# Optimization experiments

Measured on AMD Instinct MI355X. Metric: run time of the kernel, lower is better.

The kernel has to match this reference:

```python
import jax, jax.numpy as jnp
import numpy as np

N = 12000
E = 384000
F_IN, F_HID, F_OUT = 4, 50, 1433
NEG_SLOPE = 0.2  # PyG GATConv default leaky_relu slope


def gat_conv(x, W, a_src, a_dst, b, src, dst):
    """PyG GATConv (heads=1, concat=True) with self-loops already appended.
    x: [N, Fin], W: [Fin, Fout], a_src/a_dst/b: [Fout], src/dst: [E']."""
    h = x @ W                                   # [N, Fout]
    al = h @ a_src                              # [N] per-source logit part
    ar = h @ a_dst                              # [N] per-target logit part
    e = jax.nn.leaky_relu(al[src] + ar[dst], NEG_SLOPE)   # [E'] edge logits
    # segment softmax over edges grouped by destination node
    m = jax.ops.segment_max(e, dst, num_segments=N)       # [N]
    ex = jnp.exp(e - m[dst])
    s = jax.ops.segment_sum(ex, dst, num_segments=N)      # [N]
    alpha = ex / s[dst]                         # [E'] (self-loops => s > 0)
    out = jax.ops.segment_sum(alpha[:, None] * h[src], dst, num_segments=N)
    return out + b


def setup_inputs() -> dict:
    key = jax.random.key(0)
    ks = jax.random.split(key, 10)
    x = jax.random.normal(ks[0], (N, F_IN), dtype=jnp.float32)
    edge_index = jax.random.randint(ks[1], (2, E), 0, N, dtype=jnp.int32)
    # Glorot-ish init for params
    W1 = jax.random.normal(ks[2], (F_IN, F_HID), dtype=jnp.float32) / np.sqrt(F_IN)
    a_src1 = jax.random.normal(ks[3], (F_HID,), dtype=jnp.float32) / np.sqrt(F_HID)
    a_dst1 = jax.random.normal(ks[4], (F_HID,), dtype=jnp.float32) / np.sqrt(F_HID)
    b1 = jnp.zeros((F_HID,), dtype=jnp.float32)
    W2 = jax.random.normal(ks[5], (F_HID, F_OUT), dtype=jnp.float32) / np.sqrt(F_HID)
    a_src2 = jax.random.normal(ks[6], (F_OUT,), dtype=jnp.float32) / np.sqrt(F_OUT)
    a_dst2 = jax.random.normal(ks[7], (F_OUT,), dtype=jnp.float32) / np.sqrt(F_OUT)
    b2 = jnp.zeros((F_OUT,), dtype=jnp.float32)
    return {"x": x, "edge_index": edge_index, "W1": W1, "a_src1": a_src1,
            "a_dst1": a_dst1, "b1": b1, "W2": W2, "a_src2": a_src2,
            "a_dst2": a_dst2, "b2": b2}


def reference(x, edge_index, W1, a_src1, a_dst1, b1, W2, a_src2, a_dst2, b2):
    # PyG GATConv adds self-loops by default
    loops = jnp.arange(N, dtype=edge_index.dtype)
    src = jnp.concatenate([edge_index[0], loops])
    dst = jnp.concatenate([edge_index[1], loops])
    h = jax.nn.relu(gat_conv(x, W1, a_src1, a_dst1, b1, src, dst))
    h = jax.nn.relu(gat_conv(h, W2, a_src2, a_dst2, b2, src, dst))
    adj_pred = jax.nn.sigmoid(h @ h.T)          # InnerProductDecoder.forward_all
    return (adj_pred, edge_index)
```

## Files before the change

kernel.cpp:

```cpp
#include <hip/hip_runtime.h>
#include <hip/hip_bf16.h>

#define NNODES 12000
#define NEDGES 384000
#define NETOT  (NEDGES + NNODES)
#define FIN    4
#define FHID   50
#define FOUT   1433
#define KP     1440
#define MP     12032
#define NTILE  (MP / 128)
#define NTRI   (NTILE * (NTILE + 1) / 2)
#define NEG_SLOPE 0.2f

typedef __hip_bfloat16 bf16_t;
typedef __bf16 bf16x8 __attribute__((ext_vector_type(8)));
typedef float f32x4 __attribute__((ext_vector_type(4)));
typedef float f32x2 __attribute__((ext_vector_type(2)));

__device__ __forceinline__ float  b2f(bf16_t h) { return __bfloat162float(h); }
__device__ __forceinline__ bf16_t f2b(float f)  { return __float2bfloat16(f); }
__device__ __forceinline__ unsigned short f2bu(float f) { bf16_t h = f2b(f); return *(unsigned short*)&h; }

__global__ void k_init(int* __restrict__ deg, bf16_t* __restrict__ h2) {
    int i = blockIdx.x * blockDim.x + threadIdx.x;
    int stride = gridDim.x * blockDim.x;
    for (int v = i; v < NNODES; v += stride) deg[v] = 1;
    const size_t padN = (size_t)(MP - NNODES) * KP;
    for (size_t t = i; t < padN; t += stride) h2[(size_t)NNODES * KP + t] = f2b(0.f);
}

__global__ void k_count(const int* __restrict__ ei, int* __restrict__ deg) {
    int i = blockIdx.x * blockDim.x + threadIdx.x;
    if (i < NEDGES) atomicAdd(&deg[ei[NEDGES + i]], 1);
}

__global__ __launch_bounds__(1024) void k_scan(const int* __restrict__ deg,
                                               int* __restrict__ rowptr,
                                               int* __restrict__ cursor) {
    __shared__ int wsum[16];
    const int tid = threadIdx.x, lane = tid & 63, wv = tid >> 6;
    const int base = tid * 12;
    int pref[12];
    int s = 0;
#pragma unroll
    for (int u = 0; u < 12; ++u) {
        int idx = base + u;
        int d = (idx < NNODES) ? deg[idx] : 0;
        pref[u] = s;
        s += d;
    }
    int sc = s;
#pragma unroll
    for (int o = 1; o < 64; o <<= 1) {
        int t2 = __shfl_up(sc, o, 64);
        if (lane >= o) sc += t2;
    }
    if (lane == 63) wsum[wv] = sc;
    __syncthreads();
    if (wv == 0 && lane < 16) {
        int mine = wsum[lane];
        int scw = mine;
#pragma unroll
        for (int o = 1; o < 16; o <<= 1) {
            int t3 = __shfl_up(scw, o, 64);
            if (lane >= o) scw += t3;
        }
        wsum[lane] = scw - mine;
    }
    __syncthreads();
    const int pre = wsum[wv] + (sc - s);
#pragma unroll
    for (int u = 0; u < 12; ++u) {
        int idx = base + u;
        if (idx < NNODES) {
            int p = pre + pref[u];
            rowptr[idx] = p;
            cursor[idx] = p;
        }
    }
    if (tid == 1023) rowptr[NNODES] = pre + s;
}

__global__ void k_fill(const int* __restrict__ ei, int* __restrict__ cursor,
                       int* __restrict__ csrc, float* __restrict__ outbase) {
    int i = blockIdx.x * blockDim.x + threadIdx.x;
    if (i < NETOT) {
        int s, d;
        if (i < NEDGES) { s = ei[i]; d = ei[NEDGES + i]; }
        else            { s = d = i - NEDGES; }
        int pos = atomicAdd(&cursor[d], 1);
        csrc[pos] = s;
    }
    if (i < 2 * NEDGES)
        outbase[(size_t)NNODES * (size_t)NNODES + (size_t)i] = (float)ei[i];
}

__global__ __launch_bounds__(256) void k_linear1(
        const bf16_t* __restrict__ x, const bf16_t* __restrict__ W1,
        const bf16_t* __restrict__ as1, const bf16_t* __restrict__ ad1,
        float* __restrict__ h1pre, float* __restrict__ al, float* __restrict__ ar) {
    __shared__ float sW[FIN * FHID];
    __shared__ float sa[FHID], sdl[FHID];
    int tid = threadIdx.x;
    if (tid < FIN * FHID) sW[tid] = b2f(W1[tid]);
    if (tid < FHID) { sa[tid] = b2f(as1[tid]); sdl[tid] = b2f(ad1[tid]); }
    __syncthreads();
    int i = blockIdx.x * 256 + tid;
    if (i >= NNODES) return;
    float x0 = b2f(x[i * 4 + 0]), x1 = b2f(x[i * 4 + 1]);
    float x2 = b2f(x[i * 4 + 2]), x3 = b2f(x[i * 4 + 3]);
    float hal = 0.f, har = 0.f;
    for (int j = 0; j < FHID; ++j) {
        float h = x0 * sW[j] + x1 * sW[FHID + j] + x2 * sW[2 * FHID + j] + x3 * sW[3 * FHID + j];
        h1pre[(size_t)i * FHID + j] = h;
        hal += h * sa[j];
        har += h * sdl[j];
    }
    al[i] = hal; ar[i] = har;
}

__global__ __launch_bounds__(256) void k_agg1(
        const float* __restrict__ h1pre, const float* __restrict__ al, const float* __restrict__ ar,
        const int* __restrict__ rowptr, const int* __restrict__ csrc,
        const bf16_t* __restrict__ b1, float* __restrict__ h1) {
    const int wv = threadIdx.x >> 6, lane = threadIdx.x & 63;
    const int v = blockIdx.x * 4 + wv;
    const int s0 = rowptr[v], s1 = rowptr[v + 1];
    const float arv = ar[v];
    float acc = 0.f, ssum = 0.f;
    for (int base = s0; base < s1; base += 64) {
        int e = base + lane;
        float w = 0.f; int si = 0;
        if (e < s1) {
            si = csrc[e];
            float l = al[si] + arv;
            l = l > 0.f ? l : NEG_SLOPE * l;
            w = __expf(l);
        }
        ssum += w;
        int cnt = min(64, s1 - base);
#pragma unroll 4
        for (int j = 0; j < cnt; ++j) {
            float wj = __shfl(w, j, 64);
            int   sj = __shfl(si, j, 64);
            if (lane < FHID) acc += wj * h1pre[(size_t)sj * FHID + lane];
        }
    }
#pragma unroll
    for (int o = 32; o; o >>= 1) ssum += __shfl_xor(ssum, o, 64);
    if (lane < FHID) {
        float o2 = acc / ssum + b2f(b1[lane]);
        h1[(size_t)v * FHID + lane] = fmaxf(o2, 0.f);
    }
}

__global__ __launch_bounds__(256) void k_linear2(
        const float* __restrict__ h1, const bf16_t* __restrict__ W2,
        const bf16_t* __restrict__ as2, const bf16_t* __restrict__ ad2,
        unsigned char* __restrict__ h2pre, float* __restrict__ al2, float* __restrict__ ar2) {
    int v0 = blockIdx.x * 4, tid = threadIdx.x;
    __shared__ float sh[4][FHID];
    if (tid < 4 * FHID) sh[tid / FHID][tid % FHID] = h1[(size_t)v0 * FHID + tid];
    __syncthreads();
    float pal[4] = {0.f, 0.f, 0.f, 0.f}, par[4] = {0.f, 0.f, 0.f, 0.f};
#pragma unroll
    for (int i = 0; i < 3; ++i) {
        int f0 = i * 512 + 2 * tid;
        if (f0 < KP) {
            float d0[4] = {0.f, 0.f, 0.f, 0.f}, d1[4] = {0.f, 0.f, 0.f, 0.f};
            bool ok0 = f0 < FOUT, ok1 = f0 + 1 < FOUT;
            if (ok0) {
                int f1 = ok1 ? f0 + 1 : f0;
#pragma unroll 10
                for (int k = 0; k < FHID; ++k) {
                    float w0 = b2f(W2[k * FOUT + f0]);
                    float w1 = b2f(W2[k * FOUT + f1]);
#pragma unroll
                    for (int c = 0; c < 4; ++c) {
                        d0[c] += sh[c][k] * w0;
                        d1[c] += sh[c][k] * w1;
                    }
                }
                if (!ok1) { d1[0] = d1[1] = d1[2] = d1[3] = 0.f; }
                float sa0 = b2f(as2[f0]), sd0 = b2f(ad2[f0]);
                float sa1 = ok1 ? b2f(as2[f0 + 1]) : 0.f;
                float sd1 = ok1 ? b2f(ad2[f0 + 1]) : 0.f;
#pragma unroll
                for (int c = 0; c < 4; ++c) {
                    pal[c] += d0[c] * sa0 + d1[c] * sa1;
                    par[c] += d0[c] * sd0 + d1[c] * sd1;
                }
            }
#pragma unroll
            for (int c = 0; c < 4; ++c) {
                int pk = __builtin_amdgcn_cvt_pk_fp8_f32(d0[c], d1[c], 0, false);
                *(unsigned short*)(h2pre + (size_t)(v0 + c) * KP + f0) = (unsigned short)pk;
            }
        }
    }
#pragma unroll
    for (int off = 32; off; off >>= 1)
#pragma unroll
        for (int c = 0; c < 4; ++c) {
            pal[c] += __shfl_xor(pal[c], off, 64);
            par[c] += __shfl_xor(par[c], off, 64);
        }
    __shared__ float rA[4][4], rB[4][4];
    int wave = tid >> 6, lane = tid & 63;
    if (lane == 0)
#pragma unroll
        for (int c = 0; c < 4; ++c) { rA[wave][c] = pal[c]; rB[wave][c] = par[c]; }
    __syncthreads();
    if (tid < 4) {
        al2[v0 + tid] = rA[0][tid] + rA[1][tid] + rA[2][tid] + rA[3][tid];
        ar2[v0 + tid] = rB[0][tid] + rB[1][tid] + rB[2][tid] + rB[3][tid];
    }
}

__global__ __launch_bounds__(256) void k_agg2(
        const unsigned char* __restrict__ h2pre, const float* __restrict__ al, const float* __restrict__ ar,
        const int* __restrict__ rowptr, const int* __restrict__ csrc,
        const bf16_t* __restrict__ bias2, bf16_t* __restrict__ h2) {
    int v = blockIdx.x, tid = threadIdx.x;
    int s0 = rowptr[v], s1 = rowptr[v + 1];
    float arv = ar[v];
    int wave = tid >> 6, lane = tid & 63;

    float acc[8] = {0.f, 0.f, 0.f, 0.f, 0.f, 0.f, 0.f, 0.f};
    float ssum = 0.f;
    __shared__ float sw[256];
    __shared__ int ssrc[256];
    __shared__ float red[4];
    const bool act = tid < (KP / 8);
    for (int base = s0; base < s1; base += 256) {
        int e = base + tid;
        float w = 0.f; int si = 0;
        if (e < s1) {
            si = csrc[e];
            float l = al[si] + arv;
            l = l > 0.f ? l : NEG_SLOPE * l;
            w = __expf(l);
        }
        ssum += w;
        sw[tid] = w; ssrc[tid] = si;
        __syncthreads();
        int cnt = min(256, s1 - base);
        if (act) {
#pragma unroll 8
            for (int j = 0; j < cnt; ++j) {
                float wj = sw[j];
                const uint2* hp = (const uint2*)(h2pre + (size_t)ssrc[j] * KP);
                uint2 p = hp[tid];
                f32x2 e0 = __builtin_amdgcn_cvt_pk_f32_fp8(p.x, false);
                f32x2 e1 = __builtin_amdgcn_cvt_pk_f32_fp8(p.x, true);
                f32x2 e2 = __builtin_amdgcn_cvt_pk_f32_fp8(p.y, false);
                f32x2 e3 = __builtin_amdgcn_cvt_pk_f32_fp8(p.y, true);
                acc[0] += wj * e0.x; acc[1] += wj * e0.y;
                acc[2] += wj * e1.x; acc[3] += wj * e1.y;
                acc[4] += wj * e2.x; acc[5] += wj * e2.y;
                acc[6] += wj * e3.x; acc[7] += wj * e3.y;
            }
        }
        __syncthreads();
    }
#pragma unroll
    for (int off = 32; off; off >>= 1) ssum += __shfl_xor(ssum, off, 64);
    if (lane == 0) red[wave] = ssum;
    __syncthreads();
    float inv = 1.f / (red[0] + red[1] + red[2] + red[3]);

    if (act) {
        int fb = 8 * tid;
        unsigned short o[8];
#pragma unroll
        for (int t = 0; t < 8; ++t) {
            int f = fb + t;
            o[t] = f2bu((f < FOUT) ? fmaxf(acc[t] * inv + b2f(bias2[f]), 0.f) : 0.f);
        }
        uint4 pk;
        pk.x = (unsigned)o[0] | ((unsigned)o[1] << 16);
        pk.y = (unsigned)o[2] | ((unsigned)o[3] << 16);
        pk.z = (unsigned)o[4] | ((unsigned)o[5] << 16);
        pk.w = (unsigned)o[6] | ((unsigned)o[7] << 16);
        *(uint4*)(h2 + (size_t)v * KP + fb) = pk;
    }
}

__global__ __launch_bounds__(256) void k_gemm_sig(const bf16_t* __restrict__ Hm,
                                                  float* __restrict__ out) {
    int t = blockIdx.x;
    int by = (int)((2 * NTILE + 1 - sqrtf((float)(2 * NTILE + 1) * (2 * NTILE + 1) - 8.0f * t)) * 0.5f);
    if (by < 0) by = 0;
    if (by > NTILE - 1) by = NTILE - 1;
    while (by + 1 < NTILE && (by + 1) * NTILE - ((by + 1) * by) / 2 <= t) ++by;
    while (by > 0 && by * NTILE - (by * (by - 1)) / 2 > t) --by;
    int bx = by + (t - (by * NTILE - (by * (by - 1)) / 2));

    __shared__ __align__(16) bf16_t As[128 * 32];
    __shared__ __align__(16) bf16_t Bs[128 * 32];
    const int tid = threadIdx.x;
    const int wave = tid >> 6;
    const int lane = tid & 63;
    const int rowA0 = by * 128;
    const int rowB0 = bx * 128;

    const int sRow  = wave * 16 + (lane >> 2);
    const int sSlot = (lane & 3) ^ ((lane >> 2) & 3);
    const bf16_t* gA = Hm + (size_t)(rowA0 + sRow) * KP + sSlot * 8;
    const bf16_t* gB = Hm + (size_t)(rowB0 + sRow) * KP + sSlot * 8;

    f32x4 acc[4][4] = {};

    const int wrow = wave >> 1, wcol = wave & 1;
    const int r = lane & 15, q = lane >> 4;
    const int rslot = q ^ (r & 3);
    const __bf16* Asb = (const __bf16*)As;
    const __bf16* Bsb = (const __bf16*)Bs;

    for (int kt = 0; kt < KP / 32; ++kt) {
        const int k0 = kt * 32;
#pragma unroll
        for (int c = 0; c < 2; ++c) {
            __builtin_amdgcn_global_load_lds(
                (const __attribute__((address_space(1))) void*)(gA + (size_t)c * 64 * KP + k0),
                (__attribute__((address_space(3))) void*)((char*)As + c * 4096 + wave * 1024),
                16, 0, 0);
            __builtin_amdgcn_global_load_lds(
                (const __attribute__((address_space(1))) void*)(gB + (size_t)c * 64 * KP + k0),
                (__attribute__((address_space(3))) void*)((char*)Bs + c * 4096 + wave * 1024),
                16, 0, 0);
        }
        __syncthreads();
        bf16x8 af[4], bfr[4];
#pragma unroll
        for (int mi = 0; mi < 4; ++mi)
            af[mi] = *(const bf16x8*)(Asb + ((wrow * 64 + mi * 16 + r) * 32 + rslot * 8));
#pragma unroll
        for (int ni = 0; ni < 4; ++ni)
            bfr[ni] = *(const bf16x8*)(Bsb + ((wcol * 64 + ni * 16 + r) * 32 + rslot * 8));
#pragma unroll
        for (int mi = 0; mi < 4; ++mi)
#pragma unroll
            for (int ni = 0; ni < 4; ++ni)
                acc[mi][ni] = __builtin_amdgcn_mfma_f32_16x16x32_bf16(af[mi], bfr[ni], acc[mi][ni], 0, 0, 0);
        __syncthreads();
    }

#pragma unroll
    for (int mi = 0; mi < 4; ++mi) {
        const int row0 = rowA0 + wrow * 64 + mi * 16 + q * 4;
#pragma unroll
        for (int ni = 0; ni < 4; ++ni) {
            const int col = rowB0 + wcol * 64 + ni * 16 + r;
            if (col < NNODES && row0 < NNODES) {
                f32x4 s;
#pragma unroll
                for (int r2 = 0; r2 < 4; ++r2)
                    s[r2] = 1.f / (1.f + __expf(-acc[mi][ni][r2]));
#pragma unroll
                for (int r2 = 0; r2 < 4; ++r2)
                    out[(size_t)(row0 + r2) * NNODES + col] = s[r2];
                if (bx != by)
                    *(f32x4*)(out + (size_t)col * NNODES + row0) = s;
            }
        }
    }
}

extern "C" void kernel_launch(void* const* d_in, const int* in_sizes, int n_in,
                              void* d_out, int out_size, void* d_ws, size_t ws_size,
                              hipStream_t stream) {
    const bf16_t* x   = (const bf16_t*)d_in[0];
    const int*    ei  = (const int*)d_in[1];
    const bf16_t* W1  = (const bf16_t*)d_in[2];
    const bf16_t* as1 = (const bf16_t*)d_in[3];
    const bf16_t* ad1 = (const bf16_t*)d_in[4];
    const bf16_t* b1  = (const bf16_t*)d_in[5];
    const bf16_t* W2  = (const bf16_t*)d_in[6];
    const bf16_t* as2 = (const bf16_t*)d_in[7];
    const bf16_t* ad2 = (const bf16_t*)d_in[8];
    const bf16_t* b2  = (const bf16_t*)d_in[9];
    float* out = (float*)d_out;

    char* obuf = (char*)d_out;
    size_t off = 0;
    auto carve = [&](size_t bytes) {
        char* p = obuf + off;
        off += (bytes + 255) & ~(size_t)255;
        return p;
    };
    float* h1pre  = (float*)carve((size_t)NNODES * FHID * 4);
    float* al1    = (float*)carve((size_t)NNODES * 4);
    float* ar1    = (float*)carve((size_t)NNODES * 4);
    float* h1     = (float*)carve((size_t)NNODES * FHID * 4);
    float* al2    = (float*)carve((size_t)NNODES * 4);
    float* ar2    = (float*)carve((size_t)NNODES * 4);
    int*   deg    = (int*)carve((size_t)NNODES * 4);
    int*   rowptr = (int*)carve((size_t)(NNODES + 1) * 4);
    int*   cursor = (int*)carve((size_t)NNODES * 4);
    int*   csrc   = (int*)carve((size_t)NETOT * 4);
    unsigned char* h2pre = (unsigned char*)carve((size_t)NNODES * KP);
    bf16_t* h2 = (bf16_t*)d_ws;
    (void)ws_size; (void)in_sizes; (void)n_in; (void)out_size;

    hipLaunchKernelGGL(k_init,    dim3(256), dim3(256), 0, stream, deg, h2);
    hipLaunchKernelGGL(k_count,   dim3((NEDGES + 255) / 256), dim3(256), 0, stream, ei, deg);
    hipLaunchKernelGGL(k_scan,    dim3(1), dim3(1024), 0, stream, deg, rowptr, cursor);
    hipLaunchKernelGGL(k_fill,    dim3((2 * NEDGES + 255) / 256), dim3(256), 0, stream,
                       ei, cursor, csrc, out);
    hipLaunchKernelGGL(k_linear1, dim3((NNODES + 255) / 256), dim3(256), 0, stream,
                       x, W1, as1, ad1, h1pre, al1, ar1);
    hipLaunchKernelGGL(k_agg1,    dim3(NNODES / 4), dim3(256), 0, stream,
                       h1pre, al1, ar1, rowptr, csrc, b1, h1);
    hipLaunchKernelGGL(k_linear2, dim3(NNODES / 4), dim3(256), 0, stream,
                       h1, W2, as2, ad2, h2pre, al2, ar2);
    hipLaunchKernelGGL(k_agg2,    dim3(NNODES), dim3(256), 0, stream,
                       h2pre, al2, ar2, rowptr, csrc, b2, h2);
    hipLaunchKernelGGL(k_gemm_sig, dim3(NTRI), dim3(256), 0, stream, h2, out);
}
```

Baseline: 1.154 ms.

## Enlarge gram GEMM tiles to 256x256 with double-buffered async LDS pipeline

The symmetric H·Hᵀ+sigmoid GEMM now uses 256x256 output tiles with 512-thread blocks, a K-step of 64, and double-buffered LDS. The next K-tile is prefetched via global_load_lds while the current one feeds the MFMAs, using a partial vmcnt wait and raw barriers. The last 32-wide K remainder is read directly from global memory. The aim is to raise arithmetic intensity and hide global-load latency, at the cost of more registers, 128KB of LDS per block, and fewer, larger blocks (coarser triangular load balance).

```diff
diff --git a/kernel.cpp b/kernel.cpp
--- a/kernel.cpp
+++ b/kernel.cpp
@@ -9,8 +9,8 @@
 #define FOUT   1433
 #define KP     1440
 #define MP     12032
-#define NTILE  (MP / 128)
-#define NTRI   (NTILE * (NTILE + 1) / 2)
+#define GT     (MP / 256)
+#define GTRI   (GT * (GT + 1) / 2)
 #define NEG_SLOPE 0.2f
 
 typedef __hip_bfloat16 bf16_t;
@@ -287,72 +287,110 @@
     }
 }
 
-__global__ __launch_bounds__(256) void k_gemm_sig(const bf16_t* __restrict__ Hm,
-                                                  float* __restrict__ out) {
+__global__ __launch_bounds__(512, 2) void k_gemm_sig(const bf16_t* __restrict__ Hm,
+                                                     float* __restrict__ out) {
     int t = blockIdx.x;
-    int by = (int)((2 * NTILE + 1 - sqrtf((float)(2 * NTILE + 1) * (2 * NTILE + 1) - 8.0f * t)) * 0.5f);
+    int by = (int)((2 * GT + 1 - sqrtf((float)(2 * GT + 1) * (2 * GT + 1) - 8.0f * t)) * 0.5f);
     if (by < 0) by = 0;
-    if (by > NTILE - 1) by = NTILE - 1;
-    while (by + 1 < NTILE && (by + 1) * NTILE - ((by + 1) * by) / 2 <= t) ++by;
-    while (by > 0 && by * NTILE - (by * (by - 1)) / 2 > t) --by;
-    int bx = by + (t - (by * NTILE - (by * (by - 1)) / 2));
-
-    __shared__ __align__(16) bf16_t As[128 * 32];
-    __shared__ __align__(16) bf16_t Bs[128 * 32];
-    const int tid = threadIdx.x;
-    const int wave = tid >> 6;
-    const int lane = tid & 63;
-    const int rowA0 = by * 128;
-    const int rowB0 = bx * 128;
-
-    const int sRow  = wave * 16 + (lane >> 2);
-    const int sSlot = (lane & 3) ^ ((lane >> 2) & 3);
-    const bf16_t* gA = Hm + (size_t)(rowA0 + sRow) * KP + sSlot * 8;
-    const bf16_t* gB = Hm + (size_t)(rowB0 + sRow) * KP + sSlot * 8;
-
-    f32x4 acc[4][4] = {};
-
-    const int wrow = wave >> 1, wcol = wave & 1;
+    if (by > GT - 1) by = GT - 1;
+    while (by + 1 < GT && (by + 1) * GT - ((by + 1) * by) / 2 <= t) ++by;
+    while (by > 0 && by * GT - (by * (by - 1)) / 2 > t) --by;
+    int bx = by + (t - (by * GT - (by * (by - 1)) / 2));
+
+    __shared__ __align__(16) char ldsA[2 * 256 * 64 * 2];
+    __shared__ __align__(16) char ldsB[2 * 256 * 64 * 2];
+
+    const int tid  = threadIdx.x;
+    const int wave = tid >> 6, lane = tid & 63;
+    const int rowA0 = by * 256, rowB0 = bx * 256;
+
+    const int phys  = wave * 1024 + lane * 16;
+    const int physL = phys ^ (((phys >> 9) & 1) << 5);
+    const int srow  = physL >> 7;
+    const int scol  = (physL & 127) >> 1;
+    const bf16_t* gA0 = Hm + (size_t)(rowA0 + srow) * KP + scol;
+    const bf16_t* gB0 = Hm + (size_t)(rowB0 + srow) * KP + scol;
+
+#define STAGE_TILE(slot_, kt_) do {                                            \
+        char* la_ = ldsA + (slot_) * 32768 + wave * 1024;                      \
+        char* lb_ = ldsB + (slot_) * 32768 + wave * 1024;                      \
+        _Pragma("unroll")                                                      \
+        for (int c_ = 0; c_ < 4; ++c_)                                         \
+            __builtin_amdgcn_global_load_lds(                                  \
+                (const __attribute__((address_space(1))) void*)(gA0 + (size_t)(c_ * 64) * KP + (kt_) * 64), \
+                (__attribute__((address_space(3))) void*)(la_ + c_ * 8192), 16, 0, 0); \
+        _Pragma("unroll")                                                      \
+        for (int c_ = 0; c_ < 4; ++c_)                                         \
+            __builtin_amdgcn_global_load_lds(                                  \
+                (const __attribute__((address_space(1))) void*)(gB0 + (size_t)(c_ * 64) * KP + (kt_) * 64), \
+                (__attribute__((address_space(3))) void*)(lb_ + c_ * 8192), 16, 0, 0); \
+    } while (0)
+
+    const int wr = wave >> 2, wc = wave & 3;
     const int r = lane & 15, q = lane >> 4;
-    const int rslot = q ^ (r & 3);
-    const __bf16* Asb = (const __bf16*)As;
-    const __bf16* Bsb = (const __bf16*)Bs;
-
-    for (int kt = 0; kt < KP / 32; ++kt) {
-        const int k0 = kt * 32;
-#pragma unroll
-        for (int c = 0; c < 2; ++c) {
-            __builtin_amdgcn_global_load_lds(
-                (const __attribute__((address_space(1))) void*)(gA + (size_t)c * 64 * KP + k0),
-                (__attribute__((address_space(3))) void*)((char*)As + c * 4096 + wave * 1024),
-                16, 0, 0);
-            __builtin_amdgcn_global_load_lds(
-                (const __attribute__((address_space(1))) void*)(gB + (size_t)c * 64 * KP + k0),
-                (__attribute__((address_space(3))) void*)((char*)Bs + c * 4096 + wave * 1024),
-                16, 0, 0);
-        }
-        __syncthreads();
-        bf16x8 af[4], bfr[4];
-#pragma unroll
-        for (int mi = 0; mi < 4; ++mi)
-            af[mi] = *(const bf16x8*)(Asb + ((wrow * 64 + mi * 16 + r) * 32 + rslot * 8));
+    const int swz = (r & 4) << 3;
+    const int aBase = wr * 16384 + r * 128;
+    const int bBase = wc * 8192  + r * 128;
+
+    f32x4 acc[8][4] = {};
+
+    STAGE_TILE(0, 0);
+    for (int kt = 0; kt < 22; ++kt) {
+        if (kt < 21) {
+            STAGE_TILE((kt + 1) & 1, kt + 1);
+            __builtin_amdgcn_sched_barrier(0);
+            asm volatile("s_waitcnt vmcnt(8)" ::: "memory");
+        } else {
+            __builtin_amdgcn_sched_barrier(0);
+            asm volatile("s_waitcnt vmcnt(0)" ::: "memory");
+        }
+        __builtin_amdgcn_s_barrier();
+        __builtin_amdgcn_sched_barrier(0);
+        const char* Ab = ldsA + (kt & 1) * 32768;
+        const char* Bb = ldsB + (kt & 1) * 32768;
+#pragma unroll
+        for (int ks = 0; ks < 2; ++ks) {
+            const int cb = ks * 64 + ((q * 16) ^ swz);
+            bf16x8 af[8], bfr[4];
+#pragma unroll
+            for (int mi = 0; mi < 8; ++mi)
+                af[mi] = *(const bf16x8*)(Ab + aBase + mi * 2048 + cb);
+#pragma unroll
+            for (int ni = 0; ni < 4; ++ni)
+                bfr[ni] = *(const bf16x8*)(Bb + bBase + ni * 2048 + cb);
+#pragma unroll
+            for (int mi = 0; mi < 8; ++mi)
+#pragma unroll
+                for (int ni = 0; ni < 4; ++ni)
+                    acc[mi][ni] = __builtin_amdgcn_mfma_f32_16x16x32_bf16(af[mi], bfr[ni], acc[mi][ni], 0, 0, 0);
+        }
+        __builtin_amdgcn_sched_barrier(0);
+        __builtin_amdgcn_s_barrier();
+        __builtin_amdgcn_sched_barrier(0);
+    }
+#undef STAGE_TILE
+
+    {
+        bf16x8 at[8], bt[4];
+#pragma unroll
+        for (int mi = 0; mi < 8; ++mi)
+            at[mi] = *(const bf16x8*)(Hm + (size_t)(rowA0 + wr * 128 + mi * 16 + r) * KP + 1408 + q * 8);
 #pragma unroll
         for (int ni = 0; ni < 4; ++ni)
-            bfr[ni] = *(const bf16x8*)(Bsb + ((wcol * 64 + ni * 16 + r) * 32 + rslot * 8));
-#pragma unroll
-        for (int mi = 0; mi < 4; ++mi)
+            bt[ni] = *(const bf16x8*)(Hm + (size_t)(rowB0 + wc * 64 + ni * 16 + r) * KP + 1408 + q * 8);
+#pragma unroll
+        for (int mi = 0; mi < 8; ++mi)
 #pragma unroll
             for (int ni = 0; ni < 4; ++ni)
-                acc[mi][ni] = __builtin_amdgcn_mfma_f32_16x16x32_bf16(af[mi], bfr[ni], acc[mi][ni], 0, 0, 0);
-        __syncthreads();
-    }
-
-#pragma unroll
-    for (int mi = 0; mi < 4; ++mi) {
-        const int row0 = rowA0 + wrow * 64 + mi * 16 + q * 4;
+                acc[mi][ni] = __builtin_amdgcn_mfma_f32_16x16x32_bf16(at[mi], bt[ni], acc[mi][ni], 0, 0, 0);
+    }
+
+#pragma unroll
+    for (int mi = 0; mi < 8; ++mi) {
+        const int row0 = rowA0 + wr * 128 + mi * 16 + q * 4;
 #pragma unroll
         for (int ni = 0; ni < 4; ++ni) {
-            const int col = rowB0 + wcol * 64 + ni * 16 + r;
+            const int col = rowB0 + wc * 64 + ni * 16 + r;
             if (col < NNODES && row0 < NNODES) {
                 f32x4 s;
 #pragma unroll
@@ -417,5 +455,5 @@
                        h1, W2, as2, ad2, h2pre, al2, ar2);
     hipLaunchKernelGGL(k_agg2,    dim3(NNODES), dim3(256), 0, stream,
                        h2pre, al2, ar2, rowptr, csrc, b2, h2);
-    hipLaunchKernelGGL(k_gemm_sig, dim3(NTRI), dim3(256), 0, stream, h2, out);
-}
+    hipLaunchKernelGGL(k_gemm_sig, dim3(GTRI), dim3(512), 0, stream, h2, out);
+}
```

Measured after the change: 1.164 ms. About the same (+0.9%).
